# Kernel optimization log

Measured on AMD Instinct MI355X. Metric: run time of the kernel, lower is better.

Reference implementation:

```python
import jax, jax.numpy as jnp
import numpy as np

RATIO = 2
KSIZE = 12
PAD = KSIZE // 2 - RATIO // 2  # 5


def setup_inputs() -> dict:
    key = jax.random.key(0)
    k1, k2 = jax.random.split(key)
    x = jax.random.normal(k1, (4, 64, 256, 256), dtype=jnp.float32)
    # fixed anti-aliasing filter buffer (kaiser-jinc in original); random stand-in
    filt = jax.random.normal(k2, (KSIZE, KSIZE), dtype=jnp.float32)
    return {"x": x, "filt": filt}


def reference(x, filt):
    B, C, H, W = x.shape
    # reflect pad
    xp = jnp.pad(x, ((0, 0), (0, 0), (PAD, PAD), (PAD, PAD)), mode="reflect")
    # depthwise conv_transpose2d(stride=RATIO, groups=C) == conv with
    # lhs_dilation=RATIO, full padding (k-1), spatially flipped kernel
    w = jnp.broadcast_to(filt[::-1, ::-1][None, None], (C, 1, KSIZE, KSIZE))
    y = jax.lax.conv_general_dilated(
        xp, w,
        window_strides=(1, 1),
        padding=[(KSIZE - 1, KSIZE - 1)] * 2,
        lhs_dilation=(RATIO, RATIO),
        dimension_numbers=("NCHW", "OIHW", "NCHW"),
        feature_group_count=C,
    )
    y = (RATIO ** 2) * y
    pl = PAD * RATIO + (KSIZE - RATIO) // 2       # 15
    pr = PAD * RATIO + (KSIZE - RATIO + 1) // 2   # 15
    return y[..., pl:-pr, pl:-pr]
```

## Files before the change

kernel.cpp:

```cpp
#include <hip/hip_runtime.h>


#define S 40
#define WREG 576

typedef __attribute__((address_space(3))) void lds_t;
typedef __attribute__((address_space(1))) const void gm_t;

__global__ __launch_bounds__(256, 8) void upsample2d_kernel(
    const float* __restrict__ x, const float* __restrict__ filt,
    float* __restrict__ out)
{
    __shared__ float s_in[4 * WREG];

    const int tx = threadIdx.x, ty = threadIdx.y;
    const int w    = ty >> 2;
    const int lane = (ty & 3) * 16 + tx;
    const int bc  = blockIdx.z;
    const int boy = blockIdx.y, box = blockIdx.x;

    const float* xc = x + (size_t)bc * 65536;
    const int row0 = boy * 32 + w * 8 - 3;
    const int col0 = box * 32 - 3;

    float* sw = s_in + w * WREG;

    #pragma unroll
    for (int k = 0; k < 9; ++k) {
        int j = lane + 64 * k;
        int r = (j * 1639) >> 16;
        int c = j - r * 40;
        int gy = row0 + r, gx = col0 + c;
        gy = gy < 0 ? -gy : gy;  gy = gy > 255 ? 510 - gy : gy;
        gx = gx < 0 ? -gx : gx;  gx = gx > 255 ? 510 - gx : gx;
        __builtin_amdgcn_global_load_lds((gm_t*)(xc + gy * 256 + gx),
                                         (lds_t*)(sw + 64 * k), 4, 0, 0);
    }
    asm volatile("s_waitcnt vmcnt(0)" ::: "memory");

    const int xb = w * WREG + (2 * (ty & 3)) * S + 2 * tx;
    float acc[4][4] = {};
    #pragma unroll
    for (int r = 0; r < 8; ++r) {
        float xrr[8];
        #pragma unroll
        for (int cc = 0; cc < 8; ++cc) xrr[cc] = s_in[xb + r * S + cc];
        #pragma unroll
        for (int qy = 0; qy < 2; ++qy)
        #pragma unroll
        for (int py = 0; py < 2; ++py) {
            const int m = r - qy - py;
            if (m >= 0 && m <= 5) {
                #pragma unroll
                for (int px = 0; px < 2; ++px)
                #pragma unroll
                for (int n = 0; n < 6; ++n) {
                    const float f = filt[(11 - py - 2 * m) * 12 + (11 - px - 2 * n)];
                    #pragma unroll
                    for (int qx = 0; qx < 2; ++qx)
                        acc[2 * qy + py][2 * qx + px] =
                            fmaf(xrr[qx + px + n], f, acc[2 * qy + py][2 * qx + px]);
                }
            }
        }
    }

    float* oc = out + (size_t)bc * 262144;
    const int OY0 = boy * 64 + 4 * ty;
    const int OX  = box * 64 + 4 * tx;
    #pragma unroll
    for (int oy = 0; oy < 4; ++oy) {
        float4 v = make_float4(4.0f * acc[oy][0], 4.0f * acc[oy][1],
                               4.0f * acc[oy][2], 4.0f * acc[oy][3]);
        *reinterpret_cast<float4*>(&oc[(size_t)(OY0 + oy) * 512 + OX]) = v;
    }
}

extern "C" void kernel_launch(void* const* d_in, const int* in_sizes, int n_in,
                              void* d_out, int out_size, void* d_ws, size_t ws_size,
                              hipStream_t stream) {
    const float* x    = (const float*)d_in[0];
    const float* filt = (const float*)d_in[1];
    float* out = (float*)d_out;

    dim3 grid(8, 8, 256);
    dim3 block(16, 16, 1);
    upsample2d_kernel<<<grid, block, 0, stream>>>(x, filt, out);
}
```

Before: 91.93 us.

## Use packed FP32 FMA with pre-arranged filter pairs and split accumulators

A small prep kernel reorders the filter taps into pairs, with the ×4 scale folded in, and writes them to workspace. The main kernel then does its convolution with 2-wide vector FMAs, which can lower to packed FP32 instructions. Each output keeps two partial sums that are added at the end, and the separate ×4 multiply is removed. This halves the FMA instruction count, at the cost of an extra kernel launch, more accumulator registers (launch bounds drop from 8 to 6 waves) and a slightly different summation order.

```diff
diff --git a/kernel.cpp b/kernel.cpp
--- a/kernel.cpp
+++ b/kernel.cpp
@@ -4,11 +4,25 @@
 #define S 40
 #define WREG 576
 
+typedef float v2f __attribute__((ext_vector_type(2)));
 typedef __attribute__((address_space(3))) void lds_t;
 typedef __attribute__((address_space(1))) const void gm_t;
 
-__global__ __launch_bounds__(256, 8) void upsample2d_kernel(
-    const float* __restrict__ x, const float* __restrict__ filt,
+__global__ void filter_prep(const float* __restrict__ filt, float* __restrict__ ws)
+{
+    int p = threadIdx.x;
+    if (p < 72) {
+        int j = p % 3, m = (p / 3) % 6, px = (p / 18) & 1, py = p / 36;
+        int row = (11 - py - 2 * m) * 12;
+        ws[2 * p]     = 4.0f * filt[row + 11 - px - 4 * j];
+        ws[2 * p + 1] = 4.0f * filt[row + 9  - px - 4 * j];
+    }
+}
+
+#define XP(c) (((c) & 1) ? o[((c) - 1) >> 1] : e[(c) >> 1])
+
+__global__ __launch_bounds__(256, 6) void upsample2d_kernel(
+    const float* __restrict__ x, const v2f* __restrict__ ft,
     float* __restrict__ out)
 {
     __shared__ float s_in[4 * WREG];
@@ -39,12 +53,19 @@
     asm volatile("s_waitcnt vmcnt(0)" ::: "memory");
 
     const int xb = w * WREG + (2 * (ty & 3)) * S + 2 * tx;
-    float acc[4][4] = {};
+    v2f acc2[4][4] = {};
     #pragma unroll
     for (int r = 0; r < 8; ++r) {
-        float xrr[8];
+        const int rb = xb + r * S;
+        v2f e[4], o[3];
         #pragma unroll
-        for (int cc = 0; cc < 8; ++cc) xrr[cc] = s_in[xb + r * S + cc];
+        for (int j = 0; j < 4; ++j)
+            e[j] = *reinterpret_cast<const v2f*>(&s_in[rb + 2 * j]);
+        #pragma unroll
+        for (int j = 0; j < 3; ++j) {
+            o[j].x = s_in[rb + 2 * j + 1];
+            o[j].y = s_in[rb + 2 * j + 2];
+        }
         #pragma unroll
         for (int qy = 0; qy < 2; ++qy)
         #pragma unroll
@@ -52,14 +73,18 @@
             const int m = r - qy - py;
             if (m >= 0 && m <= 5) {
                 #pragma unroll
-                for (int px = 0; px < 2; ++px)
-                #pragma unroll
-                for (int n = 0; n < 6; ++n) {
-                    const float f = filt[(11 - py - 2 * m) * 12 + (11 - px - 2 * n)];
+                for (int px = 0; px < 2; ++px) {
+                    const int base = ((py * 2 + px) * 6 + m) * 3;
                     #pragma unroll
-                    for (int qx = 0; qx < 2; ++qx)
-                        acc[2 * qy + py][2 * qx + px] =
-                            fmaf(xrr[qx + px + n], f, acc[2 * qy + py][2 * qx + px]);
+                    for (int j = 0; j < 3; ++j) {
+                        const v2f f = ft[base + j];
+                        acc2[2 * qy + py][px] =
+                            __builtin_elementwise_fma(XP(px + 2 * j), f,
+                                                      acc2[2 * qy + py][px]);
+                        acc2[2 * qy + py][2 + px] =
+                            __builtin_elementwise_fma(XP(1 + px + 2 * j), f,
+                                                      acc2[2 * qy + py][2 + px]);
+                    }
                 }
             }
         }
@@ -70,8 +95,10 @@
     const int OX  = box * 64 + 4 * tx;
     #pragma unroll
     for (int oy = 0; oy < 4; ++oy) {
-        float4 v = make_float4(4.0f * acc[oy][0], 4.0f * acc[oy][1],
-                               4.0f * acc[oy][2], 4.0f * acc[oy][3]);
+        float4 v = make_float4(acc2[oy][0].x + acc2[oy][0].y,
+                               acc2[oy][1].x + acc2[oy][1].y,
+                               acc2[oy][2].x + acc2[oy][2].y,
+                               acc2[oy][3].x + acc2[oy][3].y);
         *reinterpret_cast<float4*>(&oc[(size_t)(OY0 + oy) * 512 + OX]) = v;
     }
 }
@@ -82,8 +109,11 @@
     const float* x    = (const float*)d_in[0];
     const float* filt = (const float*)d_in[1];
     float* out = (float*)d_out;
+    float* ws  = (float*)d_ws;
+
+    filter_prep<<<dim3(1), dim3(128), 0, stream>>>(filt, ws);
 
     dim3 grid(8, 8, 256);
     dim3 block(16, 16, 1);
-    upsample2d_kernel<<<grid, block, 0, stream>>>(x, filt, out);
+    upsample2d_kernel<<<grid, block, 0, stream>>>(x, (const v2f*)ws, out);
 }
```

Measured after the change: 197.4 us. +114.7%, slower.

## Use packed v2f FMA with prescaled duplicated filter table

Applied to the files above, without the earlier changes.

Adds a tiny prep kernel that flips the filter, scales it by 4 and duplicates each tap into a float2 table in workspace. The main kernel then accumulates pairs of output columns with packed two-wide FMAs (v_pk_fma_f32), building even and odd input pairs from LDS. This halves the FMA instruction count and drops the final scaling multiply. It also loosens launch bounds to 4 waves per SIMD, and it costs an extra kernel launch plus register shuffling to assemble the odd pairs.

```diff
diff --git a/kernel.cpp b/kernel.cpp
--- a/kernel.cpp
+++ b/kernel.cpp
@@ -4,11 +4,23 @@
 #define S 40
 #define WREG 576
 
+typedef float v2f __attribute__((ext_vector_type(2)));
 typedef __attribute__((address_space(3))) void lds_t;
 typedef __attribute__((address_space(1))) const void gm_t;
 
-__global__ __launch_bounds__(256, 8) void upsample2d_kernel(
-    const float* __restrict__ x, const float* __restrict__ filt,
+__global__ void filter_prep(const float* __restrict__ filt, float* __restrict__ ws)
+{
+    int t = threadIdx.x;
+    if (t < 144) {
+        int n = t % 6, m = (t / 6) % 6, px = (t / 36) & 1, py = t / 72;
+        float f = 4.0f * filt[(11 - py - 2 * m) * 12 + (11 - px - 2 * n)];
+        ws[2 * t]     = f;
+        ws[2 * t + 1] = f;
+    }
+}
+
+__global__ __launch_bounds__(256, 4) void upsample2d_kernel(
+    const float* __restrict__ x, const v2f* __restrict__ ftp,
     float* __restrict__ out)
 {
     __shared__ float s_in[4 * WREG];
@@ -39,12 +51,19 @@
     asm volatile("s_waitcnt vmcnt(0)" ::: "memory");
 
     const int xb = w * WREG + (2 * (ty & 3)) * S + 2 * tx;
-    float acc[4][4] = {};
+    v2f accp[4][2] = {};
     #pragma unroll
     for (int r = 0; r < 8; ++r) {
-        float xrr[8];
+        const int rb = xb + r * S;
+        v2f e[4], o[3];
         #pragma unroll
-        for (int cc = 0; cc < 8; ++cc) xrr[cc] = s_in[xb + r * S + cc];
+        for (int j = 0; j < 4; ++j)
+            e[j] = *reinterpret_cast<const v2f*>(&s_in[rb + 2 * j]);
+        #pragma unroll
+        for (int j = 0; j < 3; ++j) {
+            o[j].x = s_in[rb + 2 * j + 1];
+            o[j].y = s_in[rb + 2 * j + 2];
+        }
         #pragma unroll
         for (int qy = 0; qy < 2; ++qy)
         #pragma unroll
@@ -55,11 +74,11 @@
                 for (int px = 0; px < 2; ++px)
                 #pragma unroll
                 for (int n = 0; n < 6; ++n) {
-                    const float f = filt[(11 - py - 2 * m) * 12 + (11 - px - 2 * n)];
-                    #pragma unroll
-                    for (int qx = 0; qx < 2; ++qx)
-                        acc[2 * qy + py][2 * qx + px] =
-                            fmaf(xrr[qx + px + n], f, acc[2 * qy + py][2 * qx + px]);
+                    const int c = px + n;
+                    const v2f xp = (c & 1) ? o[(c - 1) >> 1] : e[c >> 1];
+                    const v2f f2 = ftp[((py * 2 + px) * 6 + m) * 6 + n];
+                    accp[2 * qy + py][px] =
+                        __builtin_elementwise_fma(xp, f2, accp[2 * qy + py][px]);
                 }
             }
         }
@@ -70,8 +89,8 @@
     const int OX  = box * 64 + 4 * tx;
     #pragma unroll
     for (int oy = 0; oy < 4; ++oy) {
-        float4 v = make_float4(4.0f * acc[oy][0], 4.0f * acc[oy][1],
-                               4.0f * acc[oy][2], 4.0f * acc[oy][3]);
+        float4 v = make_float4(accp[oy][0].x, accp[oy][1].x,
+                               accp[oy][0].y, accp[oy][1].y);
         *reinterpret_cast<float4*>(&oc[(size_t)(OY0 + oy) * 512 + OX]) = v;
     }
 }
@@ -82,8 +101,11 @@
     const float* x    = (const float*)d_in[0];
     const float* filt = (const float*)d_in[1];
     float* out = (float*)d_out;
+    float* ws  = (float*)d_ws;
+
+    filter_prep<<<dim3(1), dim3(256), 0, stream>>>(filt, ws);
 
     dim3 grid(8, 8, 256);
     dim3 block(16, 16, 1);
-    upsample2d_kernel<<<grid, block, 0, stream>>>(x, filt, out);
+    upsample2d_kernel<<<grid, block, 0, stream>>>(x, (const v2f*)ws, out);
 }
```

Measured after the change: 88.76 us. 1.04x faster.
